# Optimization experiments

Measured on AMD Instinct MI355X. Metric: run time of the kernel, lower is better.

The kernel has to match this reference:

```python
import jax, jax.numpy as jnp
import numpy as np

B, D, E, N = 2048, 4096, 512, 8192
BN_EPS = 1e-5
COS_EPS = 1e-8


def setup_inputs() -> dict:
    key = jax.random.key(0)
    k1, k2, k3, k4, k5 = jax.random.split(key, 5)
    vf = jax.random.normal(k1, (B, D), dtype=jnp.float32)
    p_wfs = jax.random.normal(k2, (B, D), dtype=jnp.float32)
    n_wfs = jax.random.normal(k3, (N, E), dtype=jnp.float32)
    # BatchNorm1d(4096) affine params (default init gamma=1, beta=0; use random-ish gamma for generality)
    gamma = jnp.ones((D,), dtype=jnp.float32)
    beta = jnp.zeros((D,), dtype=jnp.float32)
    # Linear(D -> E)
    lim = 1.0 / np.sqrt(D)
    W = jax.random.uniform(k4, (E, D), dtype=jnp.float32, minval=-lim, maxval=lim)
    b = jax.random.uniform(k5, (E,), dtype=jnp.float32, minval=-lim, maxval=lim)
    return {"vf": vf, "p_wfs": p_wfs, "n_wfs": n_wfs, "gamma": gamma, "beta": beta, "W": W, "b": b}


def _row_normalize(x, eps=COS_EPS):
    nrm = jnp.sqrt(jnp.sum(x * x, axis=-1, keepdims=True))
    return x / jnp.maximum(nrm, eps)


def reference(vf, p_wfs, n_wfs, gamma, beta, W, b):
    # BatchNorm1d in training mode: batch mean / biased variance over the batch dim
    mean = jnp.mean(vf, axis=0)
    var = jnp.mean((vf - mean) ** 2, axis=0)
    vfn = (vf - mean) * (gamma / jnp.sqrt(var + BN_EPS)) + beta  # [B, D]

    # Linear + ReLU embedding
    emb = jax.nn.relu(vfn @ W.T + b)  # [B, E]

    # p_e: row-wise cosine(normed vf, p_wfs) -> [B]
    p_e = jnp.sum(_row_normalize(vfn) * _row_normalize(p_wfs), axis=-1)

    # n_e: cosine(emb[v], n_wfs[n]) for all v,n -> one normalized GEMM [B, N]
    n_e = _row_normalize(emb) @ _row_normalize(n_wfs).T

    n_neg = n_wfs.shape[0]
    n_e_stack = n_e.reshape(-1, 1)                      # [B*N, 1]
    p_e_stack = jnp.repeat(p_e, n_neg).reshape(-1, 1)   # [B*N, 1], p_e[v] repeated N times
    return (n_e_stack, p_e_stack)
```

## Files before the change

### kernel.cpp

```cpp
#include <hip/hip_runtime.h>
#include <stdint.h>
#include <stddef.h>

#define B_ 2048
#define D_ 4096
#define E_ 512
#define N_ 8192
#define SPLITK 4

typedef unsigned short ushort_t;
typedef __attribute__((ext_vector_type(8))) short short8;
typedef __attribute__((ext_vector_type(4))) float floatx4;
typedef __attribute__((ext_vector_type(4))) unsigned short ushort4_t;

__device__ __forceinline__ void async_load16(const void* g, void* l) {
  __builtin_amdgcn_global_load_lds((__attribute__((address_space(1))) void*)(g),
                                   (__attribute__((address_space(3))) void*)(l), 16, 0, 0);
}

__device__ __forceinline__ ushort_t f2bf(float f) {
  unsigned int u = __float_as_uint(f);
  unsigned int r = (u + 0x7fffu + ((u >> 16) & 1u)) >> 16;
  return (ushort_t)r;
}
__device__ __forceinline__ float bf2f(ushort_t h) {
  return __uint_as_float(((unsigned int)h) << 16);
}

#define BAR() asm volatile("s_barrier" ::: "memory")
#define VMW(n) asm volatile("s_waitcnt vmcnt(" #n ")" ::: "memory")
#define LGKM0() asm volatile("s_waitcnt lgkmcnt(0)" ::: "memory")

__global__ __launch_bounds__(256) void bn_partial(const float* __restrict__ vf,
                                                  float* __restrict__ psum,
                                                  float* __restrict__ psq) {
  int d4 = blockIdx.x * 256 + threadIdx.x;
  int chunk = blockIdx.y;
  floatx4 s = {0.f, 0.f, 0.f, 0.f}, q = {0.f, 0.f, 0.f, 0.f};
  int r0 = chunk * 32;
  for (int r = r0; r < r0 + 32; ++r) {
    floatx4 v = ((const floatx4*)(vf + (size_t)r * D_))[d4];
    s += v; q += v * v;
  }
  ((floatx4*)(psum + (size_t)chunk * D_))[d4] = s;
  ((floatx4*)(psq  + (size_t)chunk * D_))[d4] = q;
}

__global__ __launch_bounds__(256) void prep_all(const float* __restrict__ psum,
                                                const float* __restrict__ psq,
                                                const float* __restrict__ gamma,
                                                const float* __restrict__ beta,
                                                const float* __restrict__ W,
                                                const float* __restrict__ nw,
                                                float* __restrict__ scale,
                                                float* __restrict__ shift,
                                                ushort_t* __restrict__ wb,
                                                ushort_t* __restrict__ nwb,
                                                float* __restrict__ inv_nw) {
  int bid = blockIdx.x;
  if (bid < 4) {
    int d4 = bid * 256 + threadIdx.x;
    floatx4 s = {0.f, 0.f, 0.f, 0.f}, q = {0.f, 0.f, 0.f, 0.f};
    for (int c = 0; c < 64; ++c) {
      s += ((const floatx4*)(psum + (size_t)c * D_))[d4];
      q += ((const floatx4*)(psq  + (size_t)c * D_))[d4];
    }
    floatx4 g = ((const floatx4*)gamma)[d4];
    floatx4 bt = ((const floatx4*)beta)[d4];
    floatx4 sc, sh;
#pragma unroll
    for (int j = 0; j < 4; ++j) {
      float mean = s[j] * (1.0f / B_);
      float var  = q[j] * (1.0f / B_) - mean * mean;
      float scj  = g[j] * rsqrtf(var + 1e-5f);
      sc[j] = scj;
      sh[j] = bt[j] - mean * scj;
    }
    ((floatx4*)scale)[d4] = sc;
    ((floatx4*)shift)[d4] = sh;
  } else if (bid < 2052) {
    size_t i = ((size_t)(bid - 4) * 256 + threadIdx.x) * 4;
    floatx4 x = *(const floatx4*)(W + i);
    ushort4_t o;
#pragma unroll
    for (int j = 0; j < 4; ++j) o[j] = f2bf(x[j]);
    *(ushort4_t*)(wb + i) = o;
  } else {
    int wv = threadIdx.x >> 6, l = threadIdx.x & 63;
    int n = (bid - 2052) * 4 + wv;
    const floatx4* src = (const floatx4*)(nw + (size_t)n * E_);
    ushort4_t* dst = (ushort4_t*)(nwb + (size_t)n * E_);
    float s = 0.f;
#pragma unroll
    for (int k = 0; k < 2; ++k) {
      floatx4 x = src[l + 64 * k];
      ushort4_t o;
#pragma unroll
      for (int j = 0; j < 4; ++j) { o[j] = f2bf(x[j]); s += x[j] * x[j]; }
      dst[l + 64 * k] = o;
    }
    for (int off = 32; off; off >>= 1) s += __shfl_down(s, off);
    if (l == 0) inv_nw[n] = 1.f / fmaxf(sqrtf(s), 1e-8f);
  }
}

__global__ __launch_bounds__(256) void pe_cast(const float* __restrict__ vf,
                                               const float* __restrict__ p,
                                               const float* __restrict__ scale,
                                               const float* __restrict__ shift,
                                               ushort_t* __restrict__ vfn,
                                               float* __restrict__ pe) {
  int wv = threadIdx.x >> 6, l = threadIdx.x & 63;
  int v = blockIdx.x * 4 + wv;
  const floatx4* vf4 = (const floatx4*)(vf + (size_t)v * D_);
  const floatx4* p4  = (const floatx4*)(p  + (size_t)v * D_);
  const floatx4* sc4 = (const floatx4*)scale;
  const floatx4* sh4 = (const floatx4*)shift;
  ushort_t* vrow = vfn + (size_t)v * D_;
  float sd = 0.f, sa = 0.f, sb = 0.f;
#pragma unroll 4
  for (int k = 0; k < 16; ++k) {
    int i = l + 64 * k;
    floatx4 x = vf4[i], y = p4[i], s = sc4[i], t = sh4[i];
    ushort4_t o;
#pragma unroll
    for (int j = 0; j < 4; ++j) {
      float xn = x[j] * s[j] + t[j];
      o[j] = f2bf(xn);
      sd += xn * y[j]; sa += xn * xn; sb += y[j] * y[j];
    }
    *(ushort4_t*)(vrow + i * 4) = o;
  }
  for (int off = 32; off; off >>= 1) {
    sd += __shfl_down(sd, off); sa += __shfl_down(sa, off); sb += __shfl_down(sb, off);
  }
  if (l == 0) {
    float na = fmaxf(sqrtf(sa), 1e-8f), nb = fmaxf(sqrtf(sb), 1e-8f);
    pe[v] = sd / (na * nb);
  }
}

__global__ __launch_bounds__(256, 2) void gemm1_splitk(const ushort_t* __restrict__ A,
                                                       const ushort_t* __restrict__ Bt,
                                                       float* __restrict__ partial) {
  __shared__ __align__(16) ushort_t As[2][128 * 64];
  __shared__ __align__(16) ushort_t Bs[2][64 * 64];
  floatx4 acc[4][2] = {};
  const int tid = threadIdx.x, w = tid >> 6, l = tid & 63;
  const int m16 = l & 15, q = l >> 4;
  const int wr = w >> 1, wc = w & 1;
  const int bm0 = blockIdx.y * 128, bn0 = blockIdx.x * 64;
  const int kb = blockIdx.z * (D_ / SPLITK);

  auto stageA = [&](int t, int b) {
#pragma unroll
    for (int i = 0; i < 4; ++i) {
      int lin = i * 2048 + tid * 8;
      int row = lin >> 6, colp = lin & 63;
      int col = colp ^ ((row & 7) << 3);
      async_load16(A + (size_t)(bm0 + row) * D_ + kb + t * 64 + col,
                   &As[b][i * 2048 + w * 512]);
    }
  };
  auto stageB = [&](int t, int b) {
#pragma unroll
    for (int i = 0; i < 2; ++i) {
      int lin = i * 2048 + tid * 8;
      int row = lin >> 6, colp = lin & 63;
      int col = colp ^ ((row & 7) << 3);
      async_load16(Bt + (size_t)(bn0 + row) * D_ + kb + t * 64 + col,
                   &Bs[b][i * 2048 + w * 512]);
    }
  };

  stageA(0, 0); stageB(0, 0);
  stageA(1, 1); stageB(1, 1);
  VMW(6);
  BAR();

  for (int t = 0; t < 16; ++t) {
    const int cur = t & 1;
    short8 af[4][2], bf[2][2];
#pragma unroll
    for (int i = 0; i < 4; ++i) {
      int arow = wr * 64 + i * 16 + m16;
      int sw = (arow & 7) << 3;
#pragma unroll
      for (int kc = 0; kc < 2; ++kc)
        af[i][kc] = *(const short8*)&As[cur][arow * 64 + ((kc * 32 + q * 8) ^ sw)];
    }
#pragma unroll
    for (int j = 0; j < 2; ++j) {
      int brow = wc * 32 + j * 16 + m16;
      int sw = (brow & 7) << 3;
#pragma unroll
      for (int kc = 0; kc < 2; ++kc)
        bf[j][kc] = *(const short8*)&Bs[cur][brow * 64 + ((kc * 32 + q * 8) ^ sw)];
    }
    LGKM0();
    BAR();
    if (t + 2 < 16) { stageA(t + 2, cur); stageB(t + 2, cur); }
    __builtin_amdgcn_s_setprio(1);
#pragma unroll
    for (int kc = 0; kc < 2; ++kc)
#pragma unroll
      for (int i = 0; i < 4; ++i)
#pragma unroll
        for (int j = 0; j < 2; ++j)
          acc[i][j] = __builtin_amdgcn_mfma_f32_16x16x32_bf16(af[i][kc], bf[j][kc], acc[i][j], 0, 0, 0);
    __builtin_amdgcn_s_setprio(0);
    if (t + 2 < 16) { VMW(6); } else { VMW(0); }
    BAR();
  }

  float* out = partial + (size_t)blockIdx.z * B_ * E_;
#pragma unroll
  for (int i = 0; i < 4; ++i)
#pragma unroll
    for (int j = 0; j < 2; ++j) {
      int col = bn0 + wc * 32 + j * 16 + m16;
#pragma unroll
      for (int r = 0; r < 4; ++r) {
        int row = bm0 + wr * 64 + i * 16 + q * 4 + r;
        out[(size_t)row * E_ + col] = acc[i][j][r];
      }
    }
}

__global__ __launch_bounds__(256) void gemm1_reduce(const float* __restrict__ partial,
                                                    const float* __restrict__ bias,
                                                    ushort_t* __restrict__ emb,
                                                    float* __restrict__ inv_emb) {
  int wv = threadIdx.x >> 6, l = threadIdx.x & 63;
  int row = blockIdx.x * 4 + wv;
  float sumsq = 0.f;
#pragma unroll
  for (int k = 0; k < 2; ++k) {
    int i = l + 64 * k;
    floatx4 v = {0.f, 0.f, 0.f, 0.f};
#pragma unroll
    for (int s = 0; s < SPLITK; ++s)
      v += ((const floatx4*)(partial + (size_t)s * B_ * E_ + (size_t)row * E_))[i];
    floatx4 bb = ((const floatx4*)bias)[i];
    ushort4_t o;
#pragma unroll
    for (int j = 0; j < 4; ++j) {
      float f = fmaxf(v[j] + bb[j], 0.f);
      o[j] = f2bf(f);
      float fb = bf2f(o[j]);
      sumsq += fb * fb;
    }
    ((ushort4_t*)(emb + (size_t)row * E_))[i] = o;
  }
  for (int off = 32; off; off >>= 1) sumsq += __shfl_down(sumsq, off);
  if (l == 0) inv_emb[row] = 1.f / fmaxf(sqrtf(sumsq), 1e-8f);
}

__device__ __forceinline__ void stage_A2(const ushort_t* __restrict__ A, ushort_t* Abuf,
                                         int bm0, int tk, int h, int tid) {
#pragma unroll
  for (int j = 0; j < 2; ++j) {
    int off = j * 8192 + tid * 16;
    int sl = off >> 7;
    int cb = off & 127;
    int r  = ((sl >> 6) & 1) * 128 + h * 64 + (sl & 63);
    int cg = cb ^ ((sl & 7) << 4);
    async_load16(A + (size_t)(bm0 + r) * E_ + tk * 64 + (cg >> 1),
                 Abuf + h * 8192 + j * 4096 + (tid >> 6) * 512);
  }
}

__device__ __forceinline__ void stage_B2(const ushort_t* __restrict__ Bt, ushort_t* Bbuf,
                                         int bn0, int tk, int h, int tid) {
#pragma unroll
  for (int j = 0; j < 2; ++j) {
    int off = j * 8192 + tid * 16;
    int sl = off >> 7;
    int cb = off & 127;
    int r  = ((sl >> 5) & 3) * 64 + h * 32 + (sl & 31);
    int cg = cb ^ ((sl & 7) << 4);
    async_load16(Bt + (size_t)(bn0 + r) * E_ + tk * 64 + (cg >> 1),
                 Bbuf + h * 8192 + j * 4096 + (tid >> 6) * 512);
  }
}

template <int MH, int NH>
__device__ __forceinline__ void ph_loads(const ushort_t* Ab, const ushort_t* Bb,
                                         int wr, int wc, int m16, int co0, int co1,
                                         short8 (&af)[4][2], short8 (&bfr)[2][2]) {
#pragma unroll
  for (int f = 0; f < 4; ++f) {
    const ushort_t* p = Ab + (MH * 128 + wr * 64 + f * 16 + m16) * 64;
    af[f][0] = *(const short8*)(p + co0);
    af[f][1] = *(const short8*)(p + co1);
  }
#pragma unroll
  for (int g = 0; g < 2; ++g) {
    const ushort_t* p = Bb + (NH * 128 + wc * 32 + g * 16 + m16) * 64;
    bfr[g][0] = *(const short8*)(p + co0);
    bfr[g][1] = *(const short8*)(p + co1);
  }
}

template <int MH, int NH>
__device__ __forceinline__ void ph_mma(const short8 (&af)[4][2], const short8 (&bfr)[2][2],
                                       floatx4 (&acc)[2][2][4][2]) {
  __builtin_amdgcn_s_setprio(1);
#pragma unroll
  for (int kc = 0; kc < 2; ++kc)
#pragma unroll
    for (int f = 0; f < 4; ++f)
#pragma unroll
      for (int g = 0; g < 2; ++g)
        acc[MH][NH][f][g] =
            __builtin_amdgcn_mfma_f32_16x16x32_bf16(af[f][kc], bfr[g][kc], acc[MH][NH][f][g], 0, 0, 0);
  __builtin_amdgcn_s_setprio(0);
}

__device__ __forceinline__ void out2_batch(float* __restrict__ out2, float pew,
                                           int bm0, int bn0, int b, int w, int l) {
#pragma unroll
  for (int rr = 0; rr < 4; ++rr) {
    float v = __uint_as_float(__builtin_amdgcn_readlane(__float_as_uint(pew), b * 4 + rr));
    int row = bm0 + w * 32 + b * 4 + rr;
    floatx4 vv = {v, v, v, v};
    *(floatx4*)(out2 + (size_t)row * N_ + bn0 + (l << 2)) = vv;
  }
}

#define PH(MH, NH, AB, BB, STAGE, WAIT) \
  { short8 af[4][2]; short8 bfr[2][2];                                  \
    ph_loads<MH, NH>(AB, BB, wr, wc, m16, co0, co1, af, bfr);           \
    STAGE; WAIT;                                                        \
    BAR();                                                              \
    ph_mma<MH, NH>(af, bfr, acc);                                       \
    BAR(); }

__global__ __launch_bounds__(512, 2) void gemm2_8ph(const ushort_t* __restrict__ A,
                                                    const ushort_t* __restrict__ Bt,
                                                    const float* __restrict__ inv_a,
                                                    const float* __restrict__ inv_b,
                                                    const float* __restrict__ pe,
                                                    float* __restrict__ out) {
  __shared__ __align__(16) ushort_t As_[2][16384];
  __shared__ __align__(16) ushort_t Bs_[2][16384];
  const int tid = threadIdx.x, w = tid >> 6, l = tid & 63;
  const int m16 = l & 15, q = l >> 4;
  const int wr = w >> 2, wc = w & 3;
  const int bm0 = blockIdx.y * 256, bn0 = blockIdx.x * 256;
  const int swz = (m16 & 7) << 4;
  const int co0 = ((q * 16) ^ swz) >> 1;
  const int co1 = ((64 + q * 16) ^ swz) >> 1;
  float* out2 = out + (size_t)B_ * N_;

  floatx4 acc[2][2][4][2] = {};

  float pew = pe[bm0 + w * 32 + (l & 31)];
  VMW(0);

  stage_A2(A, As_[0], bm0, 0, 0, tid);
  stage_A2(A, As_[0], bm0, 0, 1, tid);
  stage_B2(Bt, Bs_[0], bn0, 0, 0, tid);
  stage_B2(Bt, Bs_[0], bn0, 0, 1, tid);
  stage_A2(A, As_[1], bm0, 1, 0, tid);
  stage_B2(Bt, Bs_[1], bn0, 1, 0, tid);
  VMW(4);
  BAR();

#pragma unroll
  for (int i = 0; i < 4; ++i) {
    const int t1 = 2 * i + 1, t2 = 2 * i + 2, t3 = 2 * i + 3;
    const bool pre = (i < 3);
    out2_batch(out2, pew, bm0, bn0, 2 * i, w, l);
    PH(0, 0, As_[0], Bs_[0], stage_A2(A, As_[1], bm0, t1, 1, tid), ;)
    PH(0, 1, As_[0], Bs_[0], stage_B2(Bt, Bs_[1], bn0, t1, 1, tid), ;)
    PH(1, 0, As_[0], Bs_[0], if (pre) stage_A2(A, As_[0], bm0, t2, 0, tid), ;)
    PH(1, 1, As_[0], Bs_[0],
       if (pre) stage_B2(Bt, Bs_[0], bn0, t2, 0, tid),
       if (pre) { VMW(4); } else { VMW(0); })
    out2_batch(out2, pew, bm0, bn0, 2 * i + 1, w, l);
    PH(0, 0, As_[1], Bs_[1], if (pre) stage_A2(A, As_[0], bm0, t2, 1, tid), ;)
    PH(0, 1, As_[1], Bs_[1], if (pre) stage_B2(Bt, Bs_[0], bn0, t2, 1, tid), ;)
    PH(1, 0, As_[1], Bs_[1], if (pre) stage_A2(A, As_[1], bm0, t3, 0, tid), ;)
    PH(1, 1, As_[1], Bs_[1],
       if (pre) stage_B2(Bt, Bs_[1], bn0, t3, 0, tid),
       if (pre) { VMW(4); })
  }

  float ibv[2][2];
#pragma unroll
  for (int nh = 0; nh < 2; ++nh)
#pragma unroll
    for (int g = 0; g < 2; ++g)
      ibv[nh][g] = inv_b[bn0 + wc * 64 + nh * 32 + g * 16 + m16];
#pragma unroll
  for (int mh = 0; mh < 2; ++mh)
#pragma unroll
    for (int f = 0; f < 4; ++f)
#pragma unroll
      for (int rr = 0; rr < 4; ++rr) {
        int row = bm0 + wr * 128 + mh * 64 + f * 16 + q * 4 + rr;
        float ia = inv_a[row];
        size_t base = (size_t)row * N_ + bn0 + wc * 64;
#pragma unroll
        for (int nh = 0; nh < 2; ++nh)
#pragma unroll
          for (int g = 0; g < 2; ++g)
            out[base + nh * 32 + g * 16 + m16] = acc[mh][nh][f][g][rr] * ia * ibv[nh][g];
      }
}

extern "C" void kernel_launch(void* const* d_in, const int* in_sizes, int n_in,
                              void* d_out, int out_size, void* d_ws, size_t ws_size,
                              hipStream_t stream) {
  (void)in_sizes; (void)n_in; (void)out_size; (void)ws_size;
  const float* vf    = (const float*)d_in[0];
  const float* p_wfs = (const float*)d_in[1];
  const float* n_wfs = (const float*)d_in[2];
  const float* gamma = (const float*)d_in[3];
  const float* beta  = (const float*)d_in[4];
  const float* W     = (const float*)d_in[5];
  const float* bias  = (const float*)d_in[6];
  float* out = (float*)d_out;

  char* ws = (char*)d_ws;
  float* psum    = (float*)ws;  ws += (size_t)64 * D_ * 4;
  float* psq     = (float*)ws;  ws += (size_t)64 * D_ * 4;
  float* scale   = (float*)ws;  ws += (size_t)D_ * 4;
  float* shift   = (float*)ws;  ws += (size_t)D_ * 4;
  float* pe      = (float*)ws;  ws += (size_t)B_ * 4;
  float* inv_nw  = (float*)ws;  ws += (size_t)N_ * 4;
  float* inv_emb = (float*)ws;  ws += (size_t)B_ * 4;
  float* partial = (float*)ws;  ws += (size_t)SPLITK * B_ * E_ * 4;
  ushort_t* vfn  = (ushort_t*)ws;  ws += (size_t)B_ * D_ * 2;
  ushort_t* wb   = (ushort_t*)ws;  ws += (size_t)E_ * D_ * 2;
  ushort_t* nwb  = (ushort_t*)ws;  ws += (size_t)N_ * E_ * 2;
  ushort_t* emb  = (ushort_t*)ws;  ws += (size_t)B_ * E_ * 2;

  bn_partial<<<dim3(D_ / 1024, 64), 256, 0, stream>>>(vf, psum, psq);
  prep_all<<<4 + 2048 + N_ / 4, 256, 0, stream>>>(psum, psq, gamma, beta, W, n_wfs,
                                                  scale, shift, wb, nwb, inv_nw);
  pe_cast<<<B_ / 4, 256, 0, stream>>>(vf, p_wfs, scale, shift, vfn, pe);
  gemm1_splitk<<<dim3(E_ / 64, B_ / 128, SPLITK), 256, 0, stream>>>(vfn, wb, partial);
  gemm1_reduce<<<B_ / 4, 256, 0, stream>>>(partial, bias, emb, inv_emb);
  gemm2_8ph<<<dim3(N_ / 256, B_ / 256), 512, 0, stream>>>(emb, nwb, inv_emb, inv_nw, pe, out);
}
```

Before: 267.8 us.

## Fuse front-end kernels and gemm1 reduce into cooperative launches with grid sync

Merges BN partial stats, weight casts, BN finalize and the pe/cast pass into one cooperative kernel separated by grid-wide syncs. It also folds the split-K reduce into the gemm1 kernel after a grid sync. The goal is to remove several kernel launches and the gaps between them. In exchange it adds grid-barrier cost and requires every block to be co-resident; if they are not, the cooperative launch fails.

```diff
diff --git a/kernel.cpp b/kernel.cpp
--- a/kernel.cpp
+++ b/kernel.cpp
@@ -1,6 +1,9 @@
 #include <hip/hip_runtime.h>
+#include <hip/hip_cooperative_groups.h>
 #include <stdint.h>
 #include <stddef.h>
+
+namespace cg = cooperative_groups;
 
 #define B_ 2048
 #define D_ 4096
@@ -31,118 +34,114 @@
 #define VMW(n) asm volatile("s_waitcnt vmcnt(" #n ")" ::: "memory")
 #define LGKM0() asm volatile("s_waitcnt lgkmcnt(0)" ::: "memory")
 
-__global__ __launch_bounds__(256) void bn_partial(const float* __restrict__ vf,
-                                                  float* __restrict__ psum,
-                                                  float* __restrict__ psq) {
-  int d4 = blockIdx.x * 256 + threadIdx.x;
-  int chunk = blockIdx.y;
-  floatx4 s = {0.f, 0.f, 0.f, 0.f}, q = {0.f, 0.f, 0.f, 0.f};
-  int r0 = chunk * 32;
-  for (int r = r0; r < r0 + 32; ++r) {
-    floatx4 v = ((const floatx4*)(vf + (size_t)r * D_))[d4];
-    s += v; q += v * v;
-  }
-  ((floatx4*)(psum + (size_t)chunk * D_))[d4] = s;
-  ((floatx4*)(psq  + (size_t)chunk * D_))[d4] = q;
-}
-
-__global__ __launch_bounds__(256) void prep_all(const float* __restrict__ psum,
-                                                const float* __restrict__ psq,
-                                                const float* __restrict__ gamma,
-                                                const float* __restrict__ beta,
-                                                const float* __restrict__ W,
-                                                const float* __restrict__ nw,
-                                                float* __restrict__ scale,
-                                                float* __restrict__ shift,
-                                                ushort_t* __restrict__ wb,
-                                                ushort_t* __restrict__ nwb,
-                                                float* __restrict__ inv_nw) {
-  int bid = blockIdx.x;
-  if (bid < 4) {
-    int d4 = bid * 256 + threadIdx.x;
+__global__ __launch_bounds__(256, 2) void fused_front(
+    const float* __restrict__ vf, const float* __restrict__ p_wfs,
+    const float* __restrict__ gamma, const float* __restrict__ beta,
+    const float* __restrict__ W, const float* __restrict__ nw,
+    float* __restrict__ psum, float* __restrict__ psq,
+    float* __restrict__ scale, float* __restrict__ shift,
+    ushort_t* __restrict__ wb, ushort_t* __restrict__ nwb,
+    float* __restrict__ inv_nw, ushort_t* __restrict__ vfn,
+    float* __restrict__ pe) {
+  const int bid = blockIdx.x, tid = threadIdx.x;
+  const int wv = tid >> 6, l = tid & 63;
+
+  if (bid < 256) {
+    const int chunk = bid >> 2, cq = bid & 3;
+    const int d4 = cq * 256 + tid;
     floatx4 s = {0.f, 0.f, 0.f, 0.f}, q = {0.f, 0.f, 0.f, 0.f};
+    const int r0 = chunk * 32;
+    for (int r = r0; r < r0 + 32; ++r) {
+      floatx4 v = ((const floatx4*)(vf + (size_t)r * D_))[d4];
+      s += v; q += v * v;
+    }
+    ((floatx4*)(psum + (size_t)chunk * D_))[d4] = s;
+    ((floatx4*)(psq  + (size_t)chunk * D_))[d4] = q;
+  } else {
+    const int t0 = (bid - 256) * 256 + tid;
+#pragma unroll
+    for (int k = 0; k < 8; ++k) {
+      int i = t0 + k * 65536;
+      floatx4 x = ((const floatx4*)W)[i];
+      ushort4_t o;
+#pragma unroll
+      for (int j = 0; j < 4; ++j) o[j] = f2bf(x[j]);
+      ((ushort4_t*)wb)[i] = o;
+    }
+    const int w0 = (bid - 256) * 4 + wv;
+    for (int n = w0; n < N_; n += 1024) {
+      const floatx4* src = (const floatx4*)(nw + (size_t)n * E_);
+      ushort4_t* dst = (ushort4_t*)(nwb + (size_t)n * E_);
+      float s = 0.f;
+#pragma unroll
+      for (int k = 0; k < 2; ++k) {
+        floatx4 x = src[l + 64 * k];
+        ushort4_t o;
+#pragma unroll
+        for (int j = 0; j < 4; ++j) { o[j] = f2bf(x[j]); s += x[j] * x[j]; }
+        dst[l + 64 * k] = o;
+      }
+      for (int off = 32; off; off >>= 1) s += __shfl_down(s, off);
+      if (l == 0) inv_nw[n] = 1.f / fmaxf(sqrtf(s), 1e-8f);
+    }
+  }
+
+  cg::this_grid().sync();
+
+  if (bid < 16) {
+    const int col = bid * 256 + tid;
+    float s = 0.f, q = 0.f;
+#pragma unroll 8
     for (int c = 0; c < 64; ++c) {
-      s += ((const floatx4*)(psum + (size_t)c * D_))[d4];
-      q += ((const floatx4*)(psq  + (size_t)c * D_))[d4];
-    }
-    floatx4 g = ((const floatx4*)gamma)[d4];
-    floatx4 bt = ((const floatx4*)beta)[d4];
-    floatx4 sc, sh;
-#pragma unroll
-    for (int j = 0; j < 4; ++j) {
-      float mean = s[j] * (1.0f / B_);
-      float var  = q[j] * (1.0f / B_) - mean * mean;
-      float scj  = g[j] * rsqrtf(var + 1e-5f);
-      sc[j] = scj;
-      sh[j] = bt[j] - mean * scj;
-    }
-    ((floatx4*)scale)[d4] = sc;
-    ((floatx4*)shift)[d4] = sh;
-  } else if (bid < 2052) {
-    size_t i = ((size_t)(bid - 4) * 256 + threadIdx.x) * 4;
-    floatx4 x = *(const floatx4*)(W + i);
-    ushort4_t o;
-#pragma unroll
-    for (int j = 0; j < 4; ++j) o[j] = f2bf(x[j]);
-    *(ushort4_t*)(wb + i) = o;
-  } else {
-    int wv = threadIdx.x >> 6, l = threadIdx.x & 63;
-    int n = (bid - 2052) * 4 + wv;
-    const floatx4* src = (const floatx4*)(nw + (size_t)n * E_);
-    ushort4_t* dst = (ushort4_t*)(nwb + (size_t)n * E_);
-    float s = 0.f;
-#pragma unroll
-    for (int k = 0; k < 2; ++k) {
-      floatx4 x = src[l + 64 * k];
+      s += psum[(size_t)c * D_ + col];
+      q += psq[(size_t)c * D_ + col];
+    }
+    float mean = s * (1.0f / B_);
+    float var  = q * (1.0f / B_) - mean * mean;
+    float sc   = gamma[col] * rsqrtf(var + 1e-5f);
+    scale[col] = sc;
+    shift[col] = beta[col] - mean * sc;
+  }
+
+  cg::this_grid().sync();
+
+  {
+    const int v = bid * 4 + wv;
+    const floatx4* vf4 = (const floatx4*)(vf + (size_t)v * D_);
+    const floatx4* p4  = (const floatx4*)(p_wfs + (size_t)v * D_);
+    const floatx4* sc4 = (const floatx4*)scale;
+    const floatx4* sh4 = (const floatx4*)shift;
+    ushort_t* vrow = vfn + (size_t)v * D_;
+    float sd = 0.f, sa = 0.f, sb = 0.f;
+#pragma unroll 4
+    for (int k = 0; k < 16; ++k) {
+      int i = l + 64 * k;
+      floatx4 x = vf4[i], y = p4[i], s = sc4[i], t = sh4[i];
       ushort4_t o;
 #pragma unroll
-      for (int j = 0; j < 4; ++j) { o[j] = f2bf(x[j]); s += x[j] * x[j]; }
-      dst[l + 64 * k] = o;
-    }
-    for (int off = 32; off; off >>= 1) s += __shfl_down(s, off);
-    if (l == 0) inv_nw[n] = 1.f / fmaxf(sqrtf(s), 1e-8f);
-  }
-}
-
-__global__ __launch_bounds__(256) void pe_cast(const float* __restrict__ vf,
-                                               const float* __restrict__ p,
-                                               const float* __restrict__ scale,
-                                               const float* __restrict__ shift,
-                                               ushort_t* __restrict__ vfn,
-                                               float* __restrict__ pe) {
-  int wv = threadIdx.x >> 6, l = threadIdx.x & 63;
-  int v = blockIdx.x * 4 + wv;
-  const floatx4* vf4 = (const floatx4*)(vf + (size_t)v * D_);
-  const floatx4* p4  = (const floatx4*)(p  + (size_t)v * D_);
-  const floatx4* sc4 = (const floatx4*)scale;
-  const floatx4* sh4 = (const floatx4*)shift;
-  ushort_t* vrow = vfn + (size_t)v * D_;
-  float sd = 0.f, sa = 0.f, sb = 0.f;
-#pragma unroll 4
-  for (int k = 0; k < 16; ++k) {
-    int i = l + 64 * k;
-    floatx4 x = vf4[i], y = p4[i], s = sc4[i], t = sh4[i];
-    ushort4_t o;
-#pragma unroll
-    for (int j = 0; j < 4; ++j) {
-      float xn = x[j] * s[j] + t[j];
-      o[j] = f2bf(xn);
-      sd += xn * y[j]; sa += xn * xn; sb += y[j] * y[j];
-    }
-    *(ushort4_t*)(vrow + i * 4) = o;
-  }
-  for (int off = 32; off; off >>= 1) {
-    sd += __shfl_down(sd, off); sa += __shfl_down(sa, off); sb += __shfl_down(sb, off);
-  }
-  if (l == 0) {
-    float na = fmaxf(sqrtf(sa), 1e-8f), nb = fmaxf(sqrtf(sb), 1e-8f);
-    pe[v] = sd / (na * nb);
-  }
-}
-
-__global__ __launch_bounds__(256, 2) void gemm1_splitk(const ushort_t* __restrict__ A,
-                                                       const ushort_t* __restrict__ Bt,
-                                                       float* __restrict__ partial) {
+      for (int j = 0; j < 4; ++j) {
+        float xn = x[j] * s[j] + t[j];
+        o[j] = f2bf(xn);
+        sd += xn * y[j]; sa += xn * xn; sb += y[j] * y[j];
+      }
+      *(ushort4_t*)(vrow + i * 4) = o;
+    }
+    for (int off = 32; off; off >>= 1) {
+      sd += __shfl_down(sd, off); sa += __shfl_down(sa, off); sb += __shfl_down(sb, off);
+    }
+    if (l == 0) {
+      float na = fmaxf(sqrtf(sa), 1e-8f), nb = fmaxf(sqrtf(sb), 1e-8f);
+      pe[v] = sd / (na * nb);
+    }
+  }
+}
+
+__global__ __launch_bounds__(256, 2) void gemm1_fused(const ushort_t* __restrict__ A,
+                                                      const ushort_t* __restrict__ Bt,
+                                                      float* __restrict__ partial,
+                                                      const float* __restrict__ bias,
+                                                      ushort_t* __restrict__ emb,
+                                                      float* __restrict__ inv_emb) {
   __shared__ __align__(16) ushort_t As[2][128 * 64];
   __shared__ __align__(16) ushort_t Bs[2][64 * 64];
   floatx4 acc[4][2] = {};
@@ -213,47 +212,48 @@
     BAR();
   }
 
-  float* out = partial + (size_t)blockIdx.z * B_ * E_;
-#pragma unroll
-  for (int i = 0; i < 4; ++i)
-#pragma unroll
-    for (int j = 0; j < 2; ++j) {
-      int col = bn0 + wc * 32 + j * 16 + m16;
-#pragma unroll
-      for (int r = 0; r < 4; ++r) {
-        int row = bm0 + wr * 64 + i * 16 + q * 4 + r;
-        out[(size_t)row * E_ + col] = acc[i][j][r];
+  {
+    float* out = partial + (size_t)blockIdx.z * B_ * E_;
+#pragma unroll
+    for (int i = 0; i < 4; ++i)
+#pragma unroll
+      for (int j = 0; j < 2; ++j) {
+        int col = bn0 + wc * 32 + j * 16 + m16;
+#pragma unroll
+        for (int r = 0; r < 4; ++r) {
+          int row = bm0 + wr * 64 + i * 16 + q * 4 + r;
+          out[(size_t)row * E_ + col] = acc[i][j][r];
+        }
       }
-    }
-}
-
-__global__ __launch_bounds__(256) void gemm1_reduce(const float* __restrict__ partial,
-                                                    const float* __restrict__ bias,
-                                                    ushort_t* __restrict__ emb,
-                                                    float* __restrict__ inv_emb) {
-  int wv = threadIdx.x >> 6, l = threadIdx.x & 63;
-  int row = blockIdx.x * 4 + wv;
-  float sumsq = 0.f;
-#pragma unroll
-  for (int k = 0; k < 2; ++k) {
-    int i = l + 64 * k;
-    floatx4 v = {0.f, 0.f, 0.f, 0.f};
-#pragma unroll
-    for (int s = 0; s < SPLITK; ++s)
-      v += ((const floatx4*)(partial + (size_t)s * B_ * E_ + (size_t)row * E_))[i];
-    floatx4 bb = ((const floatx4*)bias)[i];
-    ushort4_t o;
-#pragma unroll
-    for (int j = 0; j < 4; ++j) {
-      float f = fmaxf(v[j] + bb[j], 0.f);
-      o[j] = f2bf(f);
-      float fb = bf2f(o[j]);
-      sumsq += fb * fb;
-    }
-    ((ushort4_t*)(emb + (size_t)row * E_))[i] = o;
-  }
-  for (int off = 32; off; off >>= 1) sumsq += __shfl_down(sumsq, off);
-  if (l == 0) inv_emb[row] = 1.f / fmaxf(sqrtf(sumsq), 1e-8f);
+  }
+
+  cg::this_grid().sync();
+
+  {
+    const int bidl = blockIdx.x + gridDim.x * (blockIdx.y + gridDim.y * blockIdx.z);
+    const int row = bidl * 4 + w;
+    float sumsq = 0.f;
+#pragma unroll
+    for (int k = 0; k < 2; ++k) {
+      int i = l + 64 * k;
+      floatx4 v = {0.f, 0.f, 0.f, 0.f};
+#pragma unroll
+      for (int s = 0; s < SPLITK; ++s)
+        v += ((const floatx4*)(partial + (size_t)s * B_ * E_ + (size_t)row * E_))[i];
+      floatx4 bb = ((const floatx4*)bias)[i];
+      ushort4_t o;
+#pragma unroll
+      for (int j = 0; j < 4; ++j) {
+        float f = fmaxf(v[j] + bb[j], 0.f);
+        o[j] = f2bf(f);
+        float fb = bf2f(o[j]);
+        sumsq += fb * fb;
+      }
+      ((ushort4_t*)(emb + (size_t)row * E_))[i] = o;
+    }
+    for (int off = 32; off; off >>= 1) sumsq += __shfl_down(sumsq, off);
+    if (l == 0) inv_emb[row] = 1.f / fmaxf(sqrtf(sumsq), 1e-8f);
+  }
 }
 
 __device__ __forceinline__ void stage_A2(const ushort_t* __restrict__ A, ushort_t* Abuf,
@@ -437,11 +437,18 @@
   ushort_t* nwb  = (ushort_t*)ws;  ws += (size_t)N_ * E_ * 2;
   ushort_t* emb  = (ushort_t*)ws;  ws += (size_t)B_ * E_ * 2;
 
-  bn_partial<<<dim3(D_ / 1024, 64), 256, 0, stream>>>(vf, psum, psq);
-  prep_all<<<4 + 2048 + N_ / 4, 256, 0, stream>>>(psum, psq, gamma, beta, W, n_wfs,
-                                                  scale, shift, wb, nwb, inv_nw);
-  pe_cast<<<B_ / 4, 256, 0, stream>>>(vf, p_wfs, scale, shift, vfn, pe);
-  gemm1_splitk<<<dim3(E_ / 64, B_ / 128, SPLITK), 256, 0, stream>>>(vfn, wb, partial);
-  gemm1_reduce<<<B_ / 4, 256, 0, stream>>>(partial, bias, emb, inv_emb);
+  {
+    void* args[] = {(void*)&vf, (void*)&p_wfs, (void*)&gamma, (void*)&beta,
+                    (void*)&W, (void*)&n_wfs, (void*)&psum, (void*)&psq,
+                    (void*)&scale, (void*)&shift, (void*)&wb, (void*)&nwb,
+                    (void*)&inv_nw, (void*)&vfn, (void*)&pe};
+    hipLaunchCooperativeKernel((void*)fused_front, dim3(512), dim3(256), args, 0, stream);
+  }
+  {
+    void* args[] = {(void*)&vfn, (void*)&wb, (void*)&partial, (void*)&bias,
+                    (void*)&emb, (void*)&inv_emb};
+    hipLaunchCooperativeKernel((void*)gemm1_fused, dim3(E_ / 64, B_ / 128, SPLITK),
+                               dim3(256), args, 0, stream);
+  }
   gemm2_8ph<<<dim3(N_ / 256, B_ / 256), 512, 0, stream>>>(emb, nwb, inv_emb, inv_nw, pe, out);
 }
```

After: 474.9 us. 1.77x slower.

## Replace split-K GEMM1 and reduce with one-pass GEMM and fused epilogue norms

Applied to the files above, without the earlier changes.

The split-K GEMM1 and its separate reduce kernel are replaced by a single full-K GEMM on 64x64 tiles. Its epilogue applies bias, ReLU and the bf16 cast, and accumulates per-row sums of squares with atomics that GEMM2 turns into inverse norms. BN partial stats are merged into the cast kernel, and a small finalize kernel computes scale/shift and zeroes the accumulator. This drops the fp32 partial-buffer round trip and two launches, at the cost of a longer K loop per block, smaller tiles with less data reuse, and order-dependent float atomics.

```diff
diff --git a/kernel.cpp b/kernel.cpp
--- a/kernel.cpp
+++ b/kernel.cpp
@@ -6,7 +6,6 @@
 #define D_ 4096
 #define E_ 512
 #define N_ 8192
-#define SPLITK 4
 
 typedef unsigned short ushort_t;
 typedef __attribute__((ext_vector_type(8))) short short8;
@@ -31,63 +30,36 @@
 #define VMW(n) asm volatile("s_waitcnt vmcnt(" #n ")" ::: "memory")
 #define LGKM0() asm volatile("s_waitcnt lgkmcnt(0)" ::: "memory")
 
-__global__ __launch_bounds__(256) void bn_partial(const float* __restrict__ vf,
+__global__ __launch_bounds__(256) void stats_cast(const float* __restrict__ vf,
+                                                  const float* __restrict__ W,
+                                                  const float* __restrict__ nw,
                                                   float* __restrict__ psum,
-                                                  float* __restrict__ psq) {
-  int d4 = blockIdx.x * 256 + threadIdx.x;
-  int chunk = blockIdx.y;
-  floatx4 s = {0.f, 0.f, 0.f, 0.f}, q = {0.f, 0.f, 0.f, 0.f};
-  int r0 = chunk * 32;
-  for (int r = r0; r < r0 + 32; ++r) {
-    floatx4 v = ((const floatx4*)(vf + (size_t)r * D_))[d4];
-    s += v; q += v * v;
-  }
-  ((floatx4*)(psum + (size_t)chunk * D_))[d4] = s;
-  ((floatx4*)(psq  + (size_t)chunk * D_))[d4] = q;
-}
-
-__global__ __launch_bounds__(256) void prep_all(const float* __restrict__ psum,
-                                                const float* __restrict__ psq,
-                                                const float* __restrict__ gamma,
-                                                const float* __restrict__ beta,
-                                                const float* __restrict__ W,
-                                                const float* __restrict__ nw,
-                                                float* __restrict__ scale,
-                                                float* __restrict__ shift,
-                                                ushort_t* __restrict__ wb,
-                                                ushort_t* __restrict__ nwb,
-                                                float* __restrict__ inv_nw) {
-  int bid = blockIdx.x;
-  if (bid < 4) {
-    int d4 = bid * 256 + threadIdx.x;
+                                                  float* __restrict__ psq,
+                                                  ushort_t* __restrict__ wb,
+                                                  ushort_t* __restrict__ nwb,
+                                                  float* __restrict__ inv_nw) {
+  const int bid = blockIdx.x, tid = threadIdx.x;
+  if (bid < 256) {
+    const int chunk = bid >> 2;
+    const int d4 = (bid & 3) * 256 + tid;
     floatx4 s = {0.f, 0.f, 0.f, 0.f}, q = {0.f, 0.f, 0.f, 0.f};
-    for (int c = 0; c < 64; ++c) {
-      s += ((const floatx4*)(psum + (size_t)c * D_))[d4];
-      q += ((const floatx4*)(psq  + (size_t)c * D_))[d4];
-    }
-    floatx4 g = ((const floatx4*)gamma)[d4];
-    floatx4 bt = ((const floatx4*)beta)[d4];
-    floatx4 sc, sh;
-#pragma unroll
-    for (int j = 0; j < 4; ++j) {
-      float mean = s[j] * (1.0f / B_);
-      float var  = q[j] * (1.0f / B_) - mean * mean;
-      float scj  = g[j] * rsqrtf(var + 1e-5f);
-      sc[j] = scj;
-      sh[j] = bt[j] - mean * scj;
-    }
-    ((floatx4*)scale)[d4] = sc;
-    ((floatx4*)shift)[d4] = sh;
-  } else if (bid < 2052) {
-    size_t i = ((size_t)(bid - 4) * 256 + threadIdx.x) * 4;
-    floatx4 x = *(const floatx4*)(W + i);
+    const int r0 = chunk * 32;
+    for (int r = r0; r < r0 + 32; ++r) {
+      floatx4 v = ((const floatx4*)(vf + (size_t)r * D_))[d4];
+      s += v; q += v * v;
+    }
+    ((floatx4*)(psum + (size_t)chunk * D_))[d4] = s;
+    ((floatx4*)(psq  + (size_t)chunk * D_))[d4] = q;
+  } else if (bid < 2304) {
+    size_t i = (size_t)(bid - 256) * 256 + tid;
+    floatx4 x = ((const floatx4*)W)[i];
     ushort4_t o;
 #pragma unroll
     for (int j = 0; j < 4; ++j) o[j] = f2bf(x[j]);
-    *(ushort4_t*)(wb + i) = o;
+    ((ushort4_t*)wb)[i] = o;
   } else {
-    int wv = threadIdx.x >> 6, l = threadIdx.x & 63;
-    int n = (bid - 2052) * 4 + wv;
+    const int wv = tid >> 6, l = tid & 63;
+    const int n = (bid - 2304) * 4 + wv;
     const floatx4* src = (const floatx4*)(nw + (size_t)n * E_);
     ushort4_t* dst = (ushort4_t*)(nwb + (size_t)n * E_);
     float s = 0.f;
@@ -102,6 +74,28 @@
     for (int off = 32; off; off >>= 1) s += __shfl_down(s, off);
     if (l == 0) inv_nw[n] = 1.f / fmaxf(sqrtf(s), 1e-8f);
   }
+}
+
+__global__ __launch_bounds__(256) void bn_finalize(const float* __restrict__ psum,
+                                                   const float* __restrict__ psq,
+                                                   const float* __restrict__ gamma,
+                                                   const float* __restrict__ beta,
+                                                   float* __restrict__ scale,
+                                                   float* __restrict__ shift,
+                                                   float* __restrict__ sumsq_e) {
+  const int col = blockIdx.x * 256 + threadIdx.x;
+  float s = 0.f, q = 0.f;
+#pragma unroll 8
+  for (int c = 0; c < 64; ++c) {
+    s += psum[(size_t)c * D_ + col];
+    q += psq[(size_t)c * D_ + col];
+  }
+  float mean = s * (1.0f / B_);
+  float var  = q * (1.0f / B_) - mean * mean;
+  float sc   = gamma[col] * rsqrtf(var + 1e-5f);
+  scale[col] = sc;
+  shift[col] = beta[col] - mean * sc;
+  if (blockIdx.x < 8) sumsq_e[blockIdx.x * 256 + threadIdx.x] = 0.f;
 }
 
 __global__ __launch_bounds__(256) void pe_cast(const float* __restrict__ vf,
@@ -140,50 +134,41 @@
   }
 }
 
-__global__ __launch_bounds__(256, 2) void gemm1_splitk(const ushort_t* __restrict__ A,
-                                                       const ushort_t* __restrict__ Bt,
-                                                       float* __restrict__ partial) {
-  __shared__ __align__(16) ushort_t As[2][128 * 64];
+__global__ __launch_bounds__(256, 2) void gemm1_onepass(const ushort_t* __restrict__ A,
+                                                        const ushort_t* __restrict__ Bt,
+                                                        const float* __restrict__ bias,
+                                                        ushort_t* __restrict__ emb,
+                                                        float* __restrict__ sumsq_e) {
+  __shared__ __align__(16) ushort_t As[2][64 * 64];
   __shared__ __align__(16) ushort_t Bs[2][64 * 64];
-  floatx4 acc[4][2] = {};
+  floatx4 acc[2][2] = {};
   const int tid = threadIdx.x, w = tid >> 6, l = tid & 63;
   const int m16 = l & 15, q = l >> 4;
   const int wr = w >> 1, wc = w & 1;
-  const int bm0 = blockIdx.y * 128, bn0 = blockIdx.x * 64;
-  const int kb = blockIdx.z * (D_ / SPLITK);
-
-  auto stageA = [&](int t, int b) {
-#pragma unroll
-    for (int i = 0; i < 4; ++i) {
-      int lin = i * 2048 + tid * 8;
-      int row = lin >> 6, colp = lin & 63;
-      int col = colp ^ ((row & 7) << 3);
-      async_load16(A + (size_t)(bm0 + row) * D_ + kb + t * 64 + col,
-                   &As[b][i * 2048 + w * 512]);
-    }
-  };
-  auto stageB = [&](int t, int b) {
+  const int bm0 = blockIdx.y * 64, bn0 = blockIdx.x * 64;
+
+  auto stageT = [&](const ushort_t* G, int r0, int t, ushort_t* buf) {
 #pragma unroll
     for (int i = 0; i < 2; ++i) {
       int lin = i * 2048 + tid * 8;
       int row = lin >> 6, colp = lin & 63;
       int col = colp ^ ((row & 7) << 3);
-      async_load16(Bt + (size_t)(bn0 + row) * D_ + kb + t * 64 + col,
-                   &Bs[b][i * 2048 + w * 512]);
+      async_load16(G + (size_t)(r0 + row) * D_ + t * 64 + col,
+                   &buf[i * 2048 + w * 512]);
     }
   };
 
-  stageA(0, 0); stageB(0, 0);
-  stageA(1, 1); stageB(1, 1);
-  VMW(6);
+  stageT(A, bm0, 0, As[0]); stageT(Bt, bn0, 0, Bs[0]);
+  stageT(A, bm0, 1, As[1]); stageT(Bt, bn0, 1, Bs[1]);
+  VMW(4);
   BAR();
 
-  for (int t = 0; t < 16; ++t) {
+  for (int t = 0; t < 64; ++t) {
     const int cur = t & 1;
-    short8 af[4][2], bf[2][2];
-#pragma unroll
-    for (int i = 0; i < 4; ++i) {
-      int arow = wr * 64 + i * 16 + m16;
+    short8 af[2][2], bf[2][2];
+#pragma unroll
+    for (int i = 0; i < 2; ++i) {
+      int arow = wr * 32 + i * 16 + m16;
       int sw = (arow & 7) << 3;
 #pragma unroll
       for (int kc = 0; kc < 2; ++kc)
@@ -199,61 +184,43 @@
     }
     LGKM0();
     BAR();
-    if (t + 2 < 16) { stageA(t + 2, cur); stageB(t + 2, cur); }
+    if (t + 2 < 64) { stageT(A, bm0, t + 2, As[cur]); stageT(Bt, bn0, t + 2, Bs[cur]); }
     __builtin_amdgcn_s_setprio(1);
 #pragma unroll
     for (int kc = 0; kc < 2; ++kc)
 #pragma unroll
-      for (int i = 0; i < 4; ++i)
+      for (int i = 0; i < 2; ++i)
 #pragma unroll
         for (int j = 0; j < 2; ++j)
           acc[i][j] = __builtin_amdgcn_mfma_f32_16x16x32_bf16(af[i][kc], bf[j][kc], acc[i][j], 0, 0, 0);
     __builtin_amdgcn_s_setprio(0);
-    if (t + 2 < 16) { VMW(6); } else { VMW(0); }
+    if (t + 2 < 64) { VMW(4); } else { VMW(0); }
     BAR();
   }
 
-  float* out = partial + (size_t)blockIdx.z * B_ * E_;
-#pragma unroll
-  for (int i = 0; i < 4; ++i)
-#pragma unroll
-    for (int j = 0; j < 2; ++j) {
-      int col = bn0 + wc * 32 + j * 16 + m16;
-#pragma unroll
-      for (int r = 0; r < 4; ++r) {
-        int row = bm0 + wr * 64 + i * 16 + q * 4 + r;
-        out[(size_t)row * E_ + col] = acc[i][j][r];
+  float bb[2];
+#pragma unroll
+  for (int j = 0; j < 2; ++j) bb[j] = bias[bn0 + wc * 32 + j * 16 + m16];
+#pragma unroll
+  for (int i = 0; i < 2; ++i)
+#pragma unroll
+    for (int r = 0; r < 4; ++r) {
+      int rowl = wr * 32 + i * 16 + q * 4 + r;
+      float ssq = 0.f;
+#pragma unroll
+      for (int j = 0; j < 2; ++j) {
+        float v = fmaxf(acc[i][j][r] + bb[j], 0.f);
+        ushort_t o = f2bf(v);
+        float fb = bf2f(o);
+        ssq += fb * fb;
+        emb[(size_t)(bm0 + rowl) * E_ + bn0 + wc * 32 + j * 16 + m16] = o;
       }
-    }
-}
-
-__global__ __launch_bounds__(256) void gemm1_reduce(const float* __restrict__ partial,
-                                                    const float* __restrict__ bias,
-                                                    ushort_t* __restrict__ emb,
-                                                    float* __restrict__ inv_emb) {
-  int wv = threadIdx.x >> 6, l = threadIdx.x & 63;
-  int row = blockIdx.x * 4 + wv;
-  float sumsq = 0.f;
-#pragma unroll
-  for (int k = 0; k < 2; ++k) {
-    int i = l + 64 * k;
-    floatx4 v = {0.f, 0.f, 0.f, 0.f};
-#pragma unroll
-    for (int s = 0; s < SPLITK; ++s)
-      v += ((const floatx4*)(partial + (size_t)s * B_ * E_ + (size_t)row * E_))[i];
-    floatx4 bb = ((const floatx4*)bias)[i];
-    ushort4_t o;
-#pragma unroll
-    for (int j = 0; j < 4; ++j) {
-      float f = fmaxf(v[j] + bb[j], 0.f);
-      o[j] = f2bf(f);
-      float fb = bf2f(o[j]);
-      sumsq += fb * fb;
-    }
-    ((ushort4_t*)(emb + (size_t)row * E_))[i] = o;
-  }
-  for (int off = 32; off; off >>= 1) sumsq += __shfl_down(sumsq, off);
-  if (l == 0) inv_emb[row] = 1.f / fmaxf(sqrtf(sumsq), 1e-8f);
+      ssq += __shfl_xor(ssq, 1);
+      ssq += __shfl_xor(ssq, 2);
+      ssq += __shfl_xor(ssq, 4);
+      ssq += __shfl_xor(ssq, 8);
+      if (m16 == 0) atomicAdd(&sumsq_e[bm0 + rowl], ssq);
+    }
 }
 
 __device__ __forceinline__ void stage_A2(const ushort_t* __restrict__ A, ushort_t* Abuf,
@@ -338,7 +305,7 @@
 
 __global__ __launch_bounds__(512, 2) void gemm2_8ph(const ushort_t* __restrict__ A,
                                                     const ushort_t* __restrict__ Bt,
-                                                    const float* __restrict__ inv_a,
+                                                    const float* __restrict__ sumsq_e,
                                                     const float* __restrict__ inv_b,
                                                     const float* __restrict__ pe,
                                                     float* __restrict__ out) {
@@ -400,7 +367,7 @@
 #pragma unroll
       for (int rr = 0; rr < 4; ++rr) {
         int row = bm0 + wr * 128 + mh * 64 + f * 16 + q * 4 + rr;
-        float ia = inv_a[row];
+        float ia = 1.f / fmaxf(sqrtf(sumsq_e[row]), 1e-8f);
         size_t base = (size_t)row * N_ + bn0 + wc * 64;
 #pragma unroll
         for (int nh = 0; nh < 2; ++nh)
@@ -430,18 +397,15 @@
   float* shift   = (float*)ws;  ws += (size_t)D_ * 4;
   float* pe      = (float*)ws;  ws += (size_t)B_ * 4;
   float* inv_nw  = (float*)ws;  ws += (size_t)N_ * 4;
-  float* inv_emb = (float*)ws;  ws += (size_t)B_ * 4;
-  float* partial = (float*)ws;  ws += (size_t)SPLITK * B_ * E_ * 4;
+  float* sumsq_e = (float*)ws;  ws += (size_t)B_ * 4;
   ushort_t* vfn  = (ushort_t*)ws;  ws += (size_t)B_ * D_ * 2;
   ushort_t* wb   = (ushort_t*)ws;  ws += (size_t)E_ * D_ * 2;
   ushort_t* nwb  = (ushort_t*)ws;  ws += (size_t)N_ * E_ * 2;
   ushort_t* emb  = (ushort_t*)ws;  ws += (size_t)B_ * E_ * 2;
 
-  bn_partial<<<dim3(D_ / 1024, 64), 256, 0, stream>>>(vf, psum, psq);
-  prep_all<<<4 + 2048 + N_ / 4, 256, 0, stream>>>(psum, psq, gamma, beta, W, n_wfs,
-                                                  scale, shift, wb, nwb, inv_nw);
+  stats_cast<<<4352, 256, 0, stream>>>(vf, W, n_wfs, psum, psq, wb, nwb, inv_nw);
+  bn_finalize<<<16, 256, 0, stream>>>(psum, psq, gamma, beta, scale, shift, sumsq_e);
   pe_cast<<<B_ / 4, 256, 0, stream>>>(vf, p_wfs, scale, shift, vfn, pe);
-  gemm1_splitk<<<dim3(E_ / 64, B_ / 128, SPLITK), 256, 0, stream>>>(vfn, wb, partial);
-  gemm1_reduce<<<B_ / 4, 256, 0, stream>>>(partial, bias, emb, inv_emb);
-  gemm2_8ph<<<dim3(N_ / 256, B_ / 256), 512, 0, stream>>>(emb, nwb, inv_emb, inv_nw, pe, out);
-}
+  gemm1_onepass<<<dim3(E_ / 64, B_ / 64), 256, 0, stream>>>(vfn, wb, bias, emb, sumsq_e);
+  gemm2_8ph<<<dim3(N_ / 256, B_ / 256), 512, 0, stream>>>(emb, nwb, sumsq_e, inv_nw, pe, out);
+}
```

New measurement: 281.7 us. 1.05x slower.
